# Kernel optimization log

Hardware: AMD Instinct MI355X
Metric: run time of the kernel (lower is better)

## Reference

```python
import jax, jax.numpy as jnp
import numpy as np

B, C, H, W = 32, 128, 64, 64
D = 256          # attn_unit_dim
FF = 512         # ffn latent dim (2.0 * 256, rounded to /16*16)
NL = 2           # n_attn_blocks
PH = PW = 2      # patch size
EPS = 1e-5


def _cf_ln(x, g, b):
    # channel-first LayerNorm over dim 1 (unbiased=False variance)
    m = jnp.mean(x, axis=1, keepdims=True)
    v = jnp.mean((x - m) ** 2, axis=1, keepdims=True)
    return (x - m) * jax.lax.rsqrt(v + EPS) * g.reshape(1, -1, 1, 1) + b.reshape(1, -1, 1, 1)


def _conv1x1(x, w, b=None):
    y = jnp.einsum('bcpq,dc->bdpq', x, w)
    return y if b is None else y + b.reshape(1, -1, 1, 1)


def _bn(x, g, b, m, v):
    # eval-mode BatchNorm2d with running stats
    return (x - m.reshape(1, -1, 1, 1)) * jax.lax.rsqrt(v.reshape(1, -1, 1, 1) + EPS) \
        * g.reshape(1, -1, 1, 1) + b.reshape(1, -1, 1, 1)


def setup_inputs() -> dict:
    key = jax.random.key(0)
    ks = iter(jax.random.split(key, 64))
    rn = lambda shape, s=0.02: jax.random.normal(next(ks), shape, jnp.float32) * s
    pv = lambda shape: 1.0 + 0.1 * jax.random.uniform(next(ks), shape, jnp.float32)
    return {
        'x': jax.random.normal(next(ks), (B, C, H, W), jnp.float32),
        # local_rep: depthwise 3x3 + BN + leaky_relu, then 1x1 -> D
        'dw_w': rn((C, 1, 3, 3), 0.1),
        'bn1_g': pv((C,)), 'bn1_b': rn((C,), 0.1),
        'bn1_m': rn((C,), 0.1), 'bn1_v': pv((C,)),
        'c1_w': rn((D, C)), 'c1_b': rn((D,), 0.01),
        # per-layer transformer params (stacked over NL)
        'ln1_g': pv((NL, D)), 'ln1_b': rn((NL, D), 0.1),
        'qkv_w': rn((NL, 1 + 2 * D, D)), 'qkv_b': rn((NL, 1 + 2 * D), 0.01),
        'out_w': rn((NL, D, D)), 'out_b': rn((NL, D), 0.01),
        'ln2_g': pv((NL, D)), 'ln2_b': rn((NL, D), 0.1),
        'f1_w': rn((NL, FF, D)), 'f1_b': rn((NL, FF), 0.01),
        'f2_w': rn((NL, D, FF)), 'f2_b': rn((NL, D), 0.01),
        'lnf_g': pv((D,)), 'lnf_b': rn((D,), 0.1),
        # conv_proj: 1x1 (no bias) + BN
        'proj_w': rn((C, D)),
        'bn2_g': pv((C,)), 'bn2_b': rn((C,), 0.1),
        'bn2_m': rn((C,), 0.1), 'bn2_v': pv((C,)),
    }


def reference(x, dw_w, bn1_g, bn1_b, bn1_m, bn1_v, c1_w, c1_b,
              ln1_g, ln1_b, qkv_w, qkv_b, out_w, out_b,
              ln2_g, ln2_b, f1_w, f1_b, f2_w, f2_b,
              lnf_g, lnf_b, proj_w, bn2_g, bn2_b, bn2_m, bn2_v):
    # local representation: depthwise 3x3 conv + BN + leaky_relu(0.1) + 1x1 conv
    y = jax.lax.conv_general_dilated(
        x, dw_w, window_strides=(1, 1), padding=[(1, 1), (1, 1)],
        dimension_numbers=('NCHW', 'OIHW', 'NCHW'), feature_group_count=C)
    y = _bn(y, bn1_g, bn1_b, bn1_m, bn1_v)
    y = jax.nn.leaky_relu(y, 0.1)
    y = _conv1x1(y, c1_w, c1_b)                       # [B, D, H, W]

    # unfold -> [B, D, P, N], P = PH*PW pixels/patch, N = patches
    nh, nw = H // PH, W // PW
    p = y.reshape(B, D, nh, PH, nw, PW).transpose(0, 1, 3, 5, 2, 4).reshape(B, D, PH * PW, nh * nw)

    # global representation: NL pre-norm linear-attention transformer blocks
    for l in range(NL):
        z = _cf_ln(p, ln1_g[l], ln1_b[l])
        qkv = _conv1x1(z, qkv_w[l], qkv_b[l])          # [B, 1+2D, P, N]
        q, k, v = qkv[:, :1], qkv[:, 1:1 + D], qkv[:, 1 + D:]
        scores = jax.nn.softmax(q, axis=-1)            # softmax over patches N
        ctx = jnp.sum(k * scores, axis=-1, keepdims=True)  # [B, D, P, 1]
        attn = _conv1x1(jax.nn.relu(v) * ctx, out_w[l], out_b[l])
        p = p + attn
        z = _cf_ln(p, ln2_g[l], ln2_b[l])
        h = jax.nn.leaky_relu(_conv1x1(z, f1_w[l], f1_b[l]), 0.1)
        p = p + _conv1x1(h, f2_w[l], f2_b[l])
    p = _cf_ln(p, lnf_g, lnf_b)

    # fold back -> [B, D, H, W]
    fm = p.reshape(B, D, PH, PW, nh, nw).transpose(0, 1, 4, 2, 5, 3).reshape(B, D, H, W)

    # conv_proj: 1x1 (no bias) + BN -> [B, C, H, W]
    fm = _conv1x1(fm, proj_w)
    fm = _bn(fm, bn2_g, bn2_b, bn2_m, bn2_v)
    return fm
```

## Files before the change

### kernel.cpp

```cpp
#include <hip/hip_runtime.h>


typedef short  bh8 __attribute__((ext_vector_type(8)));
typedef float  f4  __attribute__((ext_vector_type(4)));
typedef unsigned short us2 __attribute__((ext_vector_type(2)));
typedef unsigned short us4 __attribute__((ext_vector_type(4)));

constexpr int Bc = 32, Cc = 128, Dc = 256, FFc = 512;
constexpr int NNc = 1024, Sc = 4096;
constexpr float EPSc = 1e-5f;

enum SrcMode { S_LNF32, S_BF16 };
enum OutMode { O_STOREF32, O_FOLDBN };

__device__ __forceinline__ unsigned short f2bf(float f) {
  union { float f; unsigned int u; } v; v.f = f;
  unsigned int u = v.u + 0x7FFFu + ((v.u >> 16) & 1u);
  return (unsigned short)(u >> 16);
}

__global__ __launch_bounds__(256) void k_wconv(
    const float* __restrict__ w, unsigned short* __restrict__ dst,
    int total, int klog2)
{
  int idx = blockIdx.x * 256 + threadIdx.x;
  if (idx >= total) return;
  int K = 1 << klog2;
  int m = idx >> klog2, k = idx & (K - 1);
  int Mt = total >> klog2;
  size_t a = ((size_t)((k >> 5) * (Mt >> 4) + (m >> 4)) * 64
              + (((k >> 3) & 3) << 4) + (m & 15)) * 8 + (k & 7);
  dst[a] = f2bf(w[idx]);
}

__global__ __launch_bounds__(256) void k_dwconv(
    const float* __restrict__ x, const float* __restrict__ dww,
    const float* __restrict__ g, const float* __restrict__ bb,
    const float* __restrict__ mm, const float* __restrict__ vv,
    unsigned short* __restrict__ y1)
{
  int idx = blockIdx.x * 256 + threadIdx.x;
  int w4 = (idx & 15) * 4;
  int h  = (idx >> 4) & 63;
  int c  = (idx >> 10) & 127;
  int bi = idx >> 17;
  const float* xb = x + (size_t)(bi * 128 + c) * Sc;
  const float* wp = dww + c * 9;
  float acc[4] = {0.f, 0.f, 0.f, 0.f};
  #pragma unroll
  for (int kh = 0; kh < 3; ++kh) {
    int rr = h + kh - 1;
    if (rr < 0 || rr > 63) continue;
    const float* row = xb + rr * 64;
    float4 m4 = *reinterpret_cast<const float4*>(row + w4);
    float v[6];
    v[0] = (w4 > 0)  ? row[w4 - 1] : 0.f;
    v[1] = m4.x; v[2] = m4.y; v[3] = m4.z; v[4] = m4.w;
    v[5] = (w4 < 60) ? row[w4 + 4] : 0.f;
    float w0 = wp[kh * 3], w1 = wp[kh * 3 + 1], w2 = wp[kh * 3 + 2];
    #pragma unroll
    for (int o = 0; o < 4; ++o)
      acc[o] += w0 * v[o] + w1 * v[o + 1] + w2 * v[o + 2];
  }
  float sc = g[c] * rsqrtf(vv[c] + EPSc);
  float sh = bb[c] - mm[c] * sc;
  unsigned short r[4];
  #pragma unroll
  for (int o = 0; o < 4; ++o) {
    float val = acc[o] * sc + sh;
    r[o] = f2bf(val > 0.f ? val : 0.1f * val);
  }
  int ph = h & 1;
  size_t base = (size_t)(bi * 128 + c) * Sc + (h >> 1) * 32 + (w4 >> 1);
  *reinterpret_cast<us2*>(y1 + base + (ph * 2 + 0) * NNc) = (us2){r[0], r[2]};
  *reinterpret_cast<us2*>(y1 + base + (ph * 2 + 1) * NNc) = (us2){r[1], r[3]};
}

template<bool QD>
__global__ __launch_bounds__(256) void k_lnstats(
    const float* __restrict__ p, const float* __restrict__ wgq,
    float* __restrict__ mean_, float* __restrict__ rstd_, float* __restrict__ qdot)
{
  __shared__ float wg_s[256];
  int t = threadIdx.x;
  if (QD) { wg_s[t] = wgq[t]; __syncthreads(); }
  int pos = blockIdx.x * 256 + t;
  int b = pos >> 12, s = pos & 4095;
  const float* base = p + (size_t)b * Dc * Sc + s;
  float sum = 0.f, sq = 0.f, qa = 0.f;
  for (int d = 0; d < Dc; ++d) {
    float v = base[(size_t)d * Sc];
    sum += v; sq += v * v;
    if (QD) qa += v * wg_s[d];
  }
  float m   = sum * (1.f / Dc);
  float var = sq * (1.f / Dc) - m * m;
  mean_[pos] = m;
  rstd_[pos] = rsqrtf(fmaxf(var, 0.f) + EPSc);
  if (QD) qdot[pos] = qa;
}

__global__ void k_prep(const float* __restrict__ wq, const float* __restrict__ lng,
                       const float* __restrict__ lnb, const float* __restrict__ qb,
                       float* __restrict__ wgq, float* __restrict__ scal)
{
  int t = threadIdx.x, lane = t & 63, wv = t >> 6;
  float w = wq[t];
  float a = w * lng[t], c2 = w * lnb[t];
  wgq[t] = a;
  __shared__ float ra[4], rb[4];
  #pragma unroll
  for (int off = 32; off > 0; off >>= 1) { a += __shfl_xor(a, off); c2 += __shfl_xor(c2, off); }
  if (lane == 0) { ra[wv] = a; rb[wv] = c2; }
  __syncthreads();
  if (t == 0) {
    scal[0] = ra[0] + ra[1] + ra[2] + ra[3];
    scal[1] = rb[0] + rb[1] + rb[2] + rb[3] + qb[0];
  }
}

__global__ __launch_bounds__(256) void k_softmax2(
    const float* __restrict__ qdot, const float* __restrict__ mean_,
    const float* __restrict__ rstd_, const float* __restrict__ scal,
    float* __restrict__ ub, float* __restrict__ Ub)
{
  int bp = blockIdx.x, b = bp >> 2, pp = bp & 3;
  int t = threadIdx.x, lane = t & 63, wv = t >> 6;
  __shared__ float r3[4], r4[4];
  float s1 = scal[0], s2 = scal[1];
  int pos0 = b * Sc + pp * NNc;
  float q[4], m_r[4], rs_r[4];
  float mx = -3.4e38f;
  #pragma unroll
  for (int i = 0; i < 4; ++i) {
    int pos = pos0 + t + i * 256;
    m_r[i] = mean_[pos]; rs_r[i] = rstd_[pos];
    q[i] = rs_r[i] * qdot[pos] - m_r[i] * rs_r[i] * s1 + s2;
    mx = fmaxf(mx, q[i]);
  }
  #pragma unroll
  for (int off = 32; off > 0; off >>= 1) mx = fmaxf(mx, __shfl_xor(mx, off));
  if (lane == 0) r3[wv] = mx;
  __syncthreads();
  mx = fmaxf(fmaxf(r3[0], r3[1]), fmaxf(r3[2], r3[3]));
  float sum = 0.f;
  #pragma unroll
  for (int i = 0; i < 4; ++i) { q[i] = __expf(q[i] - mx); sum += q[i]; }
  #pragma unroll
  for (int off = 32; off > 0; off >>= 1) sum += __shfl_xor(sum, off);
  if (lane == 0) r4[wv] = sum;
  __syncthreads();
  float inv = 1.f / (r4[0] + r4[1] + r4[2] + r4[3]);
  float pU = 0.f;
  #pragma unroll
  for (int i = 0; i < 4; ++i) {
    float un = rs_r[i] * q[i] * inv;
    ub[(size_t)bp * NNc + t + i * 256] = un;
    pU += m_r[i] * un;
  }
  #pragma unroll
  for (int off = 32; off > 0; off >>= 1) pU += __shfl_xor(pU, off);
  if (lane == 0) r3[wv] = pU;
  __syncthreads();
  if (t == 0) Ub[bp] = r3[0] + r3[1] + r3[2] + r3[3];
}

__global__ __launch_bounds__(256) void k_tpass(
    const float* __restrict__ p, const float* __restrict__ ub,
    const float* __restrict__ Ub, const float* __restrict__ lng,
    const float* __restrict__ lnb, float* __restrict__ tb)
{
  int cs = blockIdx.x, pp = blockIdx.y, b = blockIdx.z;
  int bp = b * 4 + pp;
  int t = threadIdx.x, lane = t & 63, wv = t >> 6;
  __shared__ float u_s[1024];
  for (int i = t; i < 1024; i += 256) u_s[i] = ub[(size_t)bp * NNc + i];
  __syncthreads();
  float U = Ub[bp];
  const float* pb = p + (size_t)b * Dc * Sc + pp * NNc;
  for (int i = 0; i < 16; ++i) {
    int c = cs * 64 + wv * 16 + i;
    const float* row = pb + (size_t)c * Sc;
    float sm = 0.f;
    #pragma unroll
    for (int j = 0; j < 16; ++j) { int n = lane + 64 * j; sm += row[n] * u_s[n]; }
    #pragma unroll
    for (int off = 32; off > 0; off >>= 1) sm += __shfl_xor(sm, off);
    if (lane == 0) tb[(size_t)bp * Dc + c] = lng[c] * (sm - U) + lnb[c];
  }
}

__global__ __launch_bounds__(256) void k_ctx2(
    const float* __restrict__ tb, const float* __restrict__ wk,
    const float* __restrict__ bk, float* __restrict__ ctxb)
{
  int b = blockIdx.x, d = threadIdx.x;
  __shared__ float ts[4][256];
  for (int i = threadIdx.x; i < 1024; i += 256) ts[i >> 8][i & 255] = tb[(size_t)b * 1024 + i];
  __syncthreads();
  const float* wrow = wk + (size_t)d * 256;
  float bkd = bk[d];
  float accp[4] = {0.f, 0.f, 0.f, 0.f};
  for (int c = 0; c < 256; c += 4) {
    float4 wv = *reinterpret_cast<const float4*>(wrow + c);
    #pragma unroll
    for (int pp = 0; pp < 4; ++pp)
      accp[pp] += wv.x * ts[pp][c] + wv.y * ts[pp][c + 1]
                + wv.z * ts[pp][c + 2] + wv.w * ts[pp][c + 3];
  }
  #pragma unroll
  for (int pp = 0; pp < 4; ++pp)
    ctxb[((size_t)(b * 256 + d)) * 4 + pp] = accp[pp] + bkd;
}

__global__ void k_bn2pre(const float* __restrict__ g, const float* __restrict__ bb,
                         const float* __restrict__ mm, const float* __restrict__ vv,
                         float* __restrict__ sc, float* __restrict__ sh)
{
  int c = threadIdx.x;
  if (c < Cc) {
    float s = g[c] * rsqrtf(vv[c] + EPSc);
    sc[c] = s;
    sh[c] = bb[c] - mm[c] * s;
  }
}

template<int M1, bool ATTN, bool QDOT>
__global__ __launch_bounds__(256, 3) void k_fused(
    const float* __restrict__ p,
    const float* __restrict__ mean_, const float* __restrict__ rstd_,
    const float* __restrict__ lng, const float* __restrict__ lnb,
    const unsigned short* __restrict__ wf1, const float* __restrict__ b1,
    const float* __restrict__ ctxp,
    const unsigned short* __restrict__ wf2, const float* __restrict__ b2,
    float* __restrict__ dst,
    const float* __restrict__ wgq2,
    float* __restrict__ mean_o, float* __restrict__ rstd_o,
    float* __restrict__ qdot_o)
{
  constexpr int NT = 64;
  constexpr int NF = NT / 16;
  constexpr int SLABS = M1 / 128;
  int t = threadIdx.x;
  int wv = t >> 6, lane = t & 63;
  int q = lane >> 4, ln16 = lane & 15;
  int nt = blockIdx.x, pp = blockIdx.y, b = blockIdx.z;
  int n0 = nt * NT;

  __shared__ unsigned int At[256 * NT / 2];
  __shared__ unsigned short Frag[128 * NT];
  __shared__ float m_s[NT], rs_s[NT];
  __shared__ float ctx_s[ATTN ? 256 : 4];

  size_t pbase = (size_t)b * Dc * Sc + pp * NNc + n0;

  int kp_s = (t >> 5) & 7;
  int col  = (t & 31) * 2;

  auto kof = [&](int it) { return ((it >> 1) << 5) + ((it & 1) << 4) + kp_s * 2; };

  int ka = kof(0), kb = kof(1);
  float2 a0 = *reinterpret_cast<const float2*>(p + pbase + (size_t)ka * Sc + col);
  float2 a1 = *reinterpret_cast<const float2*>(p + pbase + (size_t)(ka + 1) * Sc + col);
  float2 b0 = *reinterpret_cast<const float2*>(p + pbase + (size_t)kb * Sc + col);
  float2 b1v = *reinterpret_cast<const float2*>(p + pbase + (size_t)(kb + 1) * Sc + col);

  if (t < NT) {
    int pos = b * Sc + pp * NNc + n0 + t;
    m_s[t]  = mean_[pos];
    rs_s[t] = rstd_[pos];
  }
  if (ATTN) ctx_s[t] = ctxp[(size_t)(b * Dc + t) * 4 + pp];
  __syncthreads();

  float ms0 = m_s[col], rs0 = rs_s[col];
  float ms1 = m_s[col + 1], rs1 = rs_s[col + 1];

  auto wrA = [&](int k0, int cx, unsigned int pk) {
    At[(((k0 >> 5) * 4 + (cx >> 4)) << 8) + ((((k0 >> 3) & 3) * 16 + (cx & 15)) << 2)
       + ((k0 & 7) >> 1)] = pk;
  };

  #pragma unroll 2
  for (int it = 0; it < 16; it += 2) {
    {
      int k0 = kof(it);
      float g0 = lng[k0], g1 = lng[k0 + 1];
      float h0 = lnb[k0], h1 = lnb[k0 + 1];
      float v00 = (a0.x - ms0) * rs0 * g0 + h0;
      float v01 = (a0.y - ms1) * rs1 * g0 + h0;
      float v10 = (a1.x - ms0) * rs0 * g1 + h1;
      float v11 = (a1.y - ms1) * rs1 * g1 + h1;
      if (it + 2 < 16) {
        int kn = kof(it + 2);
        a0 = *reinterpret_cast<const float2*>(p + pbase + (size_t)kn * Sc + col);
        a1 = *reinterpret_cast<const float2*>(p + pbase + (size_t)(kn + 1) * Sc + col);
      }
      wrA(k0, col,     (unsigned int)f2bf(v00) | ((unsigned int)f2bf(v10) << 16));
      wrA(k0, col + 1, (unsigned int)f2bf(v01) | ((unsigned int)f2bf(v11) << 16));
    }
    {
      int k0 = kof(it + 1);
      float g0 = lng[k0], g1 = lng[k0 + 1];
      float h0 = lnb[k0], h1 = lnb[k0 + 1];
      float v00 = (b0.x - ms0) * rs0 * g0 + h0;
      float v01 = (b0.y - ms1) * rs1 * g0 + h0;
      float v10 = (b1v.x - ms0) * rs0 * g1 + h1;
      float v11 = (b1v.y - ms1) * rs1 * g1 + h1;
      if (it + 3 < 16) {
        int kn = kof(it + 3);
        b0  = *reinterpret_cast<const float2*>(p + pbase + (size_t)kn * Sc + col);
        b1v = *reinterpret_cast<const float2*>(p + pbase + (size_t)(kn + 1) * Sc + col);
      }
      wrA(k0, col,     (unsigned int)f2bf(v00) | ((unsigned int)f2bf(v10) << 16));
      wrA(k0, col + 1, (unsigned int)f2bf(v01) | ((unsigned int)f2bf(v11) << 16));
    }
  }
  __syncthreads();

  const unsigned short* Ats = (const unsigned short*)At;

  f4 acc2[4][NF];
  #pragma unroll
  for (int i = 0; i < 4; ++i)
    #pragma unroll
    for (int j = 0; j < NF; ++j) acc2[i][j] = (f4){0.f, 0.f, 0.f, 0.f};

  for (int s = 0; s < SLABS; ++s) {
    f4 acc1[2][NF];
    #pragma unroll
    for (int i = 0; i < 2; ++i)
      #pragma unroll
      for (int j = 0; j < NF; ++j) acc1[i][j] = (f4){0.f, 0.f, 0.f, 0.f};

    for (int kc = 0; kc < 256; kc += 32) {
      bh8 aw[2];
      #pragma unroll
      for (int tm = 0; tm < 2; ++tm)
        aw[tm] = *(const bh8*)(wf1 + ((size_t)((kc >> 5) * (M1 >> 4) + s * 8 + wv * 2 + tm) * 64 + lane) * 8);
      #pragma unroll
      for (int tn = 0; tn < NF; ++tn) {
        bh8 bwf = *(const bh8*)(Ats + ((kc >> 5) * 4 + tn) * 512 + lane * 8);
        #pragma unroll
        for (int tm = 0; tm < 2; ++tm)
          acc1[tm][tn] = __builtin_amdgcn_mfma_f32_16x16x32_bf16(aw[tm], bwf, acc1[tm][tn], 0, 0, 0);
      }
    }

    __syncthreads();

    #pragma unroll
    for (int tm = 0; tm < 2; ++tm) {
      int row0l = wv * 32 + tm * 16 + q * 4;
      int row0g = s * 128 + row0l;
      float bia[4], cxv[4];
      #pragma unroll
      for (int r = 0; r < 4; ++r) {
        bia[r] = b1[row0g + r];
        if (ATTN) cxv[r] = ctx_s[row0g + r];
      }
      int kt2 = row0l >> 5;
      int sub = (row0l >> 3) & 3;
      int jo  = row0l & 7;
      #pragma unroll
      for (int tn = 0; tn < NF; ++tn) {
        int cl = tn * 16 + ln16;
        us4 pk;
        #pragma unroll
        for (int r = 0; r < 4; ++r) {
          float v = acc1[tm][tn][r] + bia[r];
          if (ATTN) v = fmaxf(v, 0.f) * cxv[r];
          else      v = v > 0.f ? v : 0.1f * v;
          pk[r] = f2bf(v);
        }
        *reinterpret_cast<us4*>(Frag + (((kt2 * 4 + (cl >> 4)) * 64 + ((sub << 4) | (cl & 15))) * 8 + jo)) = pk;
      }
    }
    __syncthreads();

    for (int kc2 = 0; kc2 < 4; ++kc2) {
      bh8 aw2[4];
      #pragma unroll
      for (int tm = 0; tm < 4; ++tm)
        aw2[tm] = *(const bh8*)(wf2 + ((size_t)((s * 4 + kc2) * 16 + wv * 4 + tm) * 64 + lane) * 8);
      #pragma unroll
      for (int tn = 0; tn < NF; ++tn) {
        bh8 bwf = *(const bh8*)(Frag + ((kc2 * 4 + tn) * 512) + lane * 8);
        #pragma unroll
        for (int tm = 0; tm < 4; ++tm)
          acc2[tm][tn] = __builtin_amdgcn_mfma_f32_16x16x32_bf16(aw2[tm], bwf, acc2[tm][tn], 0, 0, 0);
      }
    }
  }

  float s1[NF], s2[NF], s3[NF];
  #pragma unroll
  for (int tn = 0; tn < NF; ++tn) { s1[tn] = 0.f; s2[tn] = 0.f; s3[tn] = 0.f; }
  #pragma unroll
  for (int tm = 0; tm < 4; ++tm) {
    #pragma unroll
    for (int r = 0; r < 4; ++r) {
      int row = wv * 64 + tm * 16 + q * 4 + r;
      float bv = b2[row];
      float wqr = QDOT ? wgq2[row] : 0.f;
      #pragma unroll
      for (int tn = 0; tn < NF; ++tn) {
        int cx = n0 + tn * 16 + ln16;
        size_t da = (size_t)(b * Dc + row) * Sc + pp * NNc + cx;
        float v = dst[da] + acc2[tm][tn][r] + bv;
        dst[da] = v;
        s1[tn] += v; s2[tn] += v * v;
        if (QDOT) s3[tn] += v * wqr;
      }
    }
  }
  #pragma unroll
  for (int tn = 0; tn < NF; ++tn) {
    s1[tn] += __shfl_xor(s1[tn], 16); s1[tn] += __shfl_xor(s1[tn], 32);
    s2[tn] += __shfl_xor(s2[tn], 16); s2[tn] += __shfl_xor(s2[tn], 32);
    if (QDOT) { s3[tn] += __shfl_xor(s3[tn], 16); s3[tn] += __shfl_xor(s3[tn], 32); }
  }
  __syncthreads();
  float* fr = (float*)Frag;
  if (q == 0) {
    #pragma unroll
    for (int tn = 0; tn < NF; ++tn) {
      int cx = tn * 16 + ln16;
      fr[(wv * 3 + 0) * NT + cx] = s1[tn];
      fr[(wv * 3 + 1) * NT + cx] = s2[tn];
      fr[(wv * 3 + 2) * NT + cx] = s3[tn];
    }
  }
  __syncthreads();
  if (t < NT) {
    float a1s = 0.f, a2s = 0.f, a3s = 0.f;
    #pragma unroll
    for (int w2 = 0; w2 < 4; ++w2) {
      a1s += fr[(w2 * 3 + 0) * NT + t];
      a2s += fr[(w2 * 3 + 1) * NT + t];
      a3s += fr[(w2 * 3 + 2) * NT + t];
    }
    int pos = b * Sc + pp * NNc + n0 + t;
    float mn  = a1s * (1.f / 256.f);
    float var = a2s * (1.f / 256.f) - mn * mn;
    mean_o[pos] = mn;
    rstd_o[pos] = rsqrtf(fmaxf(var, 0.f) + EPSc);
    if (QDOT) qdot_o[pos] = a3s;
  }
}

template<int KTOT, int MTOT, int SRCCH, int SSTR, bool SPP,
         SrcMode SM, OutMode OM>
__global__ __launch_bounds__(256) void k_mm(
    const void* __restrict__ src,
    const float* __restrict__ mean_, const float* __restrict__ rstd_,
    const float* __restrict__ lng, const float* __restrict__ lnb,
    const unsigned short* __restrict__ wf, const float* __restrict__ bias,
    const float* __restrict__ bnsc, const float* __restrict__ bnsh,
    void* __restrict__ dst)
{
  int t = threadIdx.x;
  int wv = t >> 6, lane = t & 63;
  int wm = wv & 1, wn = wv >> 1;
  int q = lane >> 4, ln16 = lane & 15;
  int nb = blockIdx.x, b = blockIdx.z;
  int pp = blockIdx.y & 3, mb = blockIdx.y >> 2;
  int n0  = nb * 128;
  int MB0 = mb * 128;

  __shared__ unsigned int Alds[128 * 20];
  __shared__ float m_s[128], rs_s[128];

  if (SM == S_LNF32 && t < 128) {
    int pos = b * Sc + pp * NNc + n0 + t;
    m_s[t]  = mean_[pos];
    rs_s[t] = rstd_[pos];
  }

  f4 acc[4][4];
  #pragma unroll
  for (int i = 0; i < 4; ++i)
    #pragma unroll
    for (int j = 0; j < 4; ++j) acc[i][j] = (f4){0.f, 0.f, 0.f, 0.f};

  size_t sbase = (size_t)b * SRCCH * SSTR + pp * NNc + n0;
  int mtb = (MB0 >> 4) + wm * 4;

  for (int kc = 0; kc < KTOT; kc += 32) {
    bh8 aw[4];
    #pragma unroll
    for (int tm = 0; tm < 4; ++tm)
      aw[tm] = *(const bh8*)(wf + ((size_t)((kc >> 5) * (MTOT >> 4) + mtb + tm) * 64 + lane) * 8);
    __syncthreads();
    #pragma unroll
    for (int it = 0; it < 8; ++it) {
      int n_l = (t & 63) + (it & 1) * 64;
      int kp  = (t >> 6) + (it >> 1) * 4;
      int k0  = kc + kp * 2;
      unsigned int pk;
      if (SM == S_LNF32) {
        const float* sp = (const float*)src;
        float a0 = sp[sbase + (size_t)k0 * SSTR + n_l];
        float a1 = sp[sbase + (size_t)(k0 + 1) * SSTR + n_l];
        float ms = m_s[n_l], rs = rs_s[n_l];
        a0 = (a0 - ms) * rs * lng[k0] + lnb[k0];
        a1 = (a1 - ms) * rs * lng[k0 + 1] + lnb[k0 + 1];
        pk = (unsigned int)f2bf(a0) | ((unsigned int)f2bf(a1) << 16);
      } else {
        const unsigned short* sp = (const unsigned short*)src;
        unsigned int u0 = sp[sbase + (size_t)k0 * SSTR + n_l];
        unsigned int u1 = sp[sbase + (size_t)(k0 + 1) * SSTR + n_l];
        pk = u0 | (u1 << 16);
      }
      Alds[n_l * 20 + kp] = pk;
    }
    __syncthreads();
    const unsigned short* al = (const unsigned short*)Alds;
    #pragma unroll
    for (int tn = 0; tn < 4; ++tn) {
      int nrow = wn * 64 + tn * 16 + ln16;
      bh8 bwf = *(const bh8*)(al + nrow * 40 + q * 8);
      #pragma unroll
      for (int tm = 0; tm < 4; ++tm)
        acc[tm][tn] = __builtin_amdgcn_mfma_f32_16x16x32_bf16(aw[tm], bwf, acc[tm][tn], 0, 0, 0);
    }
  }

  #pragma unroll
  for (int tm = 0; tm < 4; ++tm) {
    #pragma unroll
    for (int r = 0; r < 4; ++r) {
      int row = MB0 + wm * 64 + tm * 16 + q * 4 + r;
      float scv = 0.f, shv = 0.f, bv = 0.f;
      if (OM == O_FOLDBN) { scv = bnsc[row]; shv = bnsh[row]; }
      else                { bv = bias[row]; }
      #pragma unroll
      for (int tn = 0; tn < 4; ++tn) {
        int col = n0 + wn * 64 + tn * 16 + ln16;
        float v = acc[tm][tn][r];
        if (OM == O_FOLDBN) {
          int hh = 2 * (col >> 5) + (pp >> 1), ww = 2 * (col & 31) + (pp & 1);
          ((float*)dst)[((size_t)(b * Cc + row)) * Sc + hh * 64 + ww] = v * scv + shv;
        } else {
          ((float*)dst)[(size_t)(b * MTOT + row) * Sc + pp * NNc + col] = v + bv;
        }
      }
    }
  }
}

extern "C" void kernel_launch(void* const* d_in, const int* in_sizes, int n_in,
                              void* d_out, int out_size, void* d_ws, size_t ws_size,
                              hipStream_t stream)
{
  const float* x     = (const float*)d_in[0];
  const float* dw_w  = (const float*)d_in[1];
  const float* bn1_g = (const float*)d_in[2];
  const float* bn1_b = (const float*)d_in[3];
  const float* bn1_m = (const float*)d_in[4];
  const float* bn1_v = (const float*)d_in[5];
  const float* c1_w  = (const float*)d_in[6];
  const float* c1_b  = (const float*)d_in[7];
  const float* ln1_g = (const float*)d_in[8];
  const float* ln1_b = (const float*)d_in[9];
  const float* qkv_w = (const float*)d_in[10];
  const float* qkv_b = (const float*)d_in[11];
  const float* out_w = (const float*)d_in[12];
  const float* out_b = (const float*)d_in[13];
  const float* ln2_g = (const float*)d_in[14];
  const float* ln2_b = (const float*)d_in[15];
  const float* f1_w  = (const float*)d_in[16];
  const float* f1_b  = (const float*)d_in[17];
  const float* f2_w  = (const float*)d_in[18];
  const float* f2_b  = (const float*)d_in[19];
  const float* lnf_g = (const float*)d_in[20];
  const float* lnf_b = (const float*)d_in[21];
  const float* projw = (const float*)d_in[22];
  const float* bn2_g = (const float*)d_in[23];
  const float* bn2_b = (const float*)d_in[24];
  const float* bn2_m = (const float*)d_in[25];
  const float* bn2_v = (const float*)d_in[26];
  float* out = (float*)d_out;

  float* ws    = (float*)d_ws;
  float* p     = ws;
  float* reg   = p + (size_t)33554432;
  unsigned short* y1u = (unsigned short*)reg;
  float* mean2 = reg;
  float* rstd2 = reg + 131072;
  float* meanb = reg   + (size_t)8388608;
  float* rstdb = meanb + 131072;
  float* qdotb = rstdb + 131072;
  float* ub    = qdotb + 131072;
  float* Ub    = ub    + 131072;
  float* tb    = Ub    + 128;
  float* ctxb  = tb    + 32768;
  float* wgq   = ctxb  + 32768;
  float* scal  = wgq   + 512;
  float* bnscb = scal  + 16;
  float* bnshb = bnscb + 128;
  unsigned short* wfb = (unsigned short*)(bnshb + 128);
  unsigned short* wf_c1   = wfb;
  unsigned short* wf_v0   = wfb + 32768;
  unsigned short* wf_proj = wfb + 32768 + 2 * 393216;

  k_wconv<<<128, 256, 0, stream>>>(c1_w, wf_c1, 256 * 128, 7);
  for (int l = 0; l < 2; ++l) {
    const float* wvp = qkv_w + ((size_t)l * 513 + 257) * Dc;
    unsigned short* base = wf_v0 + (size_t)l * 393216;
    k_wconv<<<256, 256, 0, stream>>>(wvp, base, 256 * 256, 8);
    k_wconv<<<256, 256, 0, stream>>>(out_w + (size_t)l * Dc * Dc, base + 65536, 256 * 256, 8);
    k_wconv<<<512, 256, 0, stream>>>(f1_w + (size_t)l * FFc * Dc, base + 131072, 512 * 256, 8);
    k_wconv<<<512, 256, 0, stream>>>(f2_w + (size_t)l * Dc * FFc, base + 262144, 256 * 512, 9);
  }
  k_wconv<<<128, 256, 0, stream>>>(projw, wf_proj, 128 * 256, 8);

  for (int l = 0; l < 2; ++l)
    k_prep<<<1, 256, 0, stream>>>(qkv_w + (size_t)l * 513 * Dc,
                                  ln1_g + l * Dc, ln1_b + l * Dc,
                                  qkv_b + l * 513, wgq + l * 256, scal + l * 2);

  k_dwconv<<<16384, 256, 0, stream>>>(x, dw_w, bn1_g, bn1_b, bn1_m, bn1_v, y1u);

  k_mm<128, 256, 128, 4096, true, S_BF16, O_STOREF32>
      <<<dim3(8, 8, 32), 256, 0, stream>>>(
      y1u, nullptr, nullptr, nullptr, nullptr, wf_c1, c1_b, nullptr, nullptr, p);

  k_lnstats<true><<<512, 256, 0, stream>>>(p, wgq, meanb, rstdb, qdotb);

  for (int l = 0; l < 2; ++l) {
    const float* g1 = ln1_g + l * Dc; const float* b1 = ln1_b + l * Dc;
    const float* g2 = ln2_g + l * Dc; const float* b2 = ln2_b + l * Dc;
    const float* wk = qkv_w + ((size_t)l * 513 + 1) * Dc;
    const float* bk = qkv_b + l * 513 + 1;
    const float* bvv = qkv_b + l * 513 + 257;
    unsigned short* wbase = wf_v0 + (size_t)l * 393216;

    k_softmax2<<<128, 256, 0, stream>>>(qdotb, meanb, rstdb, scal + l * 2, ub, Ub);
    k_tpass<<<dim3(4, 4, 32), 256, 0, stream>>>(p, ub, Ub, g1, b1, tb);
    k_ctx2<<<32, 256, 0, stream>>>(tb, wk, bk, ctxb);

    k_fused<256, true, false><<<dim3(16, 4, 32), 256, 0, stream>>>(
        p, meanb, rstdb, g1, b1, wbase, bvv, ctxb,
        wbase + 65536, out_b + l * Dc, p,
        nullptr, mean2, rstd2, nullptr);

    if (l == 0) {
      k_fused<512, false, true><<<dim3(16, 4, 32), 256, 0, stream>>>(
          p, mean2, rstd2, g2, b2, wbase + 131072, f1_b + l * FFc, nullptr,
          wbase + 262144, f2_b + l * Dc, p,
          wgq + 256, meanb, rstdb, qdotb);
    } else {
      k_fused<512, false, false><<<dim3(16, 4, 32), 256, 0, stream>>>(
          p, mean2, rstd2, g2, b2, wbase + 131072, f1_b + l * FFc, nullptr,
          wbase + 262144, f2_b + l * Dc, p,
          nullptr, meanb, rstdb, nullptr);
    }
  }

  k_bn2pre<<<1, 128, 0, stream>>>(bn2_g, bn2_b, bn2_m, bn2_v, bnscb, bnshb);
  k_mm<256, 128, 256, 4096, true, S_LNF32, O_FOLDBN>
      <<<dim3(8, 4, 32), 256, 0, stream>>>(
      p, meanb, rstdb, lnf_g, lnf_b, wf_proj, nullptr, bnscb, bnshb, out);
}
```

Measured before the change: 878.3 us.

## Use 512-thread blocks in fused MLP kernel and prefetch residual early

Doubles the fused attention/FFN kernel's block to 8 waves. Each wave now owns half as many output rows in both GEMMs, and the layernorm staging loop runs half as many iterations per thread. The residual values from p are loaded into registers before the GEMM loop, so the epilogue no longer does a read-modify-write from global memory. This is meant to raise waves per CU and hide latency. In exchange, the block needs more barrier participation, the cross-wave reduction grows to 8 partials, and holding the residuals adds register pressure.

```diff
diff --git a/kernel.cpp b/kernel.cpp
--- a/kernel.cpp
+++ b/kernel.cpp
@@ -226,7 +226,7 @@
 }
 
 template<int M1, bool ATTN, bool QDOT>
-__global__ __launch_bounds__(256, 3) void k_fused(
+__global__ __launch_bounds__(512, 4) void k_fused(
     const float* __restrict__ p,
     const float* __restrict__ mean_, const float* __restrict__ rstd_,
     const float* __restrict__ lng, const float* __restrict__ lnb,
@@ -254,10 +254,10 @@
 
   size_t pbase = (size_t)b * Dc * Sc + pp * NNc + n0;
 
-  int kp_s = (t >> 5) & 7;
+  int kp_s = t >> 5;
   int col  = (t & 31) * 2;
 
-  auto kof = [&](int it) { return ((it >> 1) << 5) + ((it & 1) << 4) + kp_s * 2; };
+  auto kof = [&](int it) { return (it << 5) + kp_s * 2; };
 
   int ka = kof(0), kb = kof(1);
   float2 a0 = *reinterpret_cast<const float2*>(p + pbase + (size_t)ka * Sc + col);
@@ -270,7 +270,7 @@
     m_s[t]  = mean_[pos];
     rs_s[t] = rstd_[pos];
   }
-  if (ATTN) ctx_s[t] = ctxp[(size_t)(b * Dc + t) * 4 + pp];
+  if (ATTN && t < 256) ctx_s[t] = ctxp[(size_t)(b * Dc + t) * 4 + pp];
   __syncthreads();
 
   float ms0 = m_s[col], rs0 = rs_s[col];
@@ -281,8 +281,8 @@
        + ((k0 & 7) >> 1)] = pk;
   };
 
-  #pragma unroll 2
-  for (int it = 0; it < 16; it += 2) {
+  #pragma unroll
+  for (int it = 0; it < 8; it += 2) {
     {
       int k0 = kof(it);
       float g0 = lng[k0], g1 = lng[k0 + 1];
@@ -291,7 +291,7 @@
       float v01 = (a0.y - ms1) * rs1 * g0 + h0;
       float v10 = (a1.x - ms0) * rs0 * g1 + h1;
       float v11 = (a1.y - ms1) * rs1 * g1 + h1;
-      if (it + 2 < 16) {
+      if (it + 2 < 8) {
         int kn = kof(it + 2);
         a0 = *reinterpret_cast<const float2*>(p + pbase + (size_t)kn * Sc + col);
         a1 = *reinterpret_cast<const float2*>(p + pbase + (size_t)(kn + 1) * Sc + col);
@@ -307,7 +307,7 @@
       float v01 = (b0.y - ms1) * rs1 * g0 + h0;
       float v10 = (b1v.x - ms0) * rs0 * g1 + h1;
       float v11 = (b1v.y - ms1) * rs1 * g1 + h1;
-      if (it + 3 < 16) {
+      if (it + 3 < 8) {
         int kn = kof(it + 3);
         b0  = *reinterpret_cast<const float2*>(p + pbase + (size_t)kn * Sc + col);
         b1v = *reinterpret_cast<const float2*>(p + pbase + (size_t)(kn + 1) * Sc + col);
@@ -318,40 +318,43 @@
   }
   __syncthreads();
 
+  float res[2][4][4];
+  #pragma unroll
+  for (int tm = 0; tm < 2; ++tm)
+    #pragma unroll
+    for (int r = 0; r < 4; ++r) {
+      int row = wv * 32 + tm * 16 + q * 4 + r;
+      #pragma unroll
+      for (int tn = 0; tn < NF; ++tn)
+        res[tm][r][tn] = dst[pbase + (size_t)row * Sc + tn * 16 + ln16];
+    }
+
   const unsigned short* Ats = (const unsigned short*)At;
 
-  f4 acc2[4][NF];
-  #pragma unroll
-  for (int i = 0; i < 4; ++i)
+  f4 acc2[2][NF];
+  #pragma unroll
+  for (int i = 0; i < 2; ++i)
     #pragma unroll
     for (int j = 0; j < NF; ++j) acc2[i][j] = (f4){0.f, 0.f, 0.f, 0.f};
 
   for (int s = 0; s < SLABS; ++s) {
-    f4 acc1[2][NF];
-    #pragma unroll
-    for (int i = 0; i < 2; ++i)
-      #pragma unroll
-      for (int j = 0; j < NF; ++j) acc1[i][j] = (f4){0.f, 0.f, 0.f, 0.f};
+    f4 acc1[NF];
+    #pragma unroll
+    for (int j = 0; j < NF; ++j) acc1[j] = (f4){0.f, 0.f, 0.f, 0.f};
 
     for (int kc = 0; kc < 256; kc += 32) {
-      bh8 aw[2];
-      #pragma unroll
-      for (int tm = 0; tm < 2; ++tm)
-        aw[tm] = *(const bh8*)(wf1 + ((size_t)((kc >> 5) * (M1 >> 4) + s * 8 + wv * 2 + tm) * 64 + lane) * 8);
+      bh8 aw = *(const bh8*)(wf1 + ((size_t)((kc >> 5) * (M1 >> 4) + s * 8 + wv) * 64 + lane) * 8);
       #pragma unroll
       for (int tn = 0; tn < NF; ++tn) {
         bh8 bwf = *(const bh8*)(Ats + ((kc >> 5) * 4 + tn) * 512 + lane * 8);
-        #pragma unroll
-        for (int tm = 0; tm < 2; ++tm)
-          acc1[tm][tn] = __builtin_amdgcn_mfma_f32_16x16x32_bf16(aw[tm], bwf, acc1[tm][tn], 0, 0, 0);
+        acc1[tn] = __builtin_amdgcn_mfma_f32_16x16x32_bf16(aw, bwf, acc1[tn], 0, 0, 0);
       }
     }
 
     __syncthreads();
 
-    #pragma unroll
-    for (int tm = 0; tm < 2; ++tm) {
-      int row0l = wv * 32 + tm * 16 + q * 4;
+    {
+      int row0l = wv * 16 + q * 4;
       int row0g = s * 128 + row0l;
       float bia[4], cxv[4];
       #pragma unroll
@@ -368,7 +371,7 @@
         us4 pk;
         #pragma unroll
         for (int r = 0; r < 4; ++r) {
-          float v = acc1[tm][tn][r] + bia[r];
+          float v = acc1[tn][r] + bia[r];
           if (ATTN) v = fmaxf(v, 0.f) * cxv[r];
           else      v = v > 0.f ? v : 0.1f * v;
           pk[r] = f2bf(v);
@@ -379,15 +382,15 @@
     __syncthreads();
 
     for (int kc2 = 0; kc2 < 4; ++kc2) {
-      bh8 aw2[4];
-      #pragma unroll
-      for (int tm = 0; tm < 4; ++tm)
-        aw2[tm] = *(const bh8*)(wf2 + ((size_t)((s * 4 + kc2) * 16 + wv * 4 + tm) * 64 + lane) * 8);
+      bh8 aw2[2];
+      #pragma unroll
+      for (int tm = 0; tm < 2; ++tm)
+        aw2[tm] = *(const bh8*)(wf2 + ((size_t)((s * 4 + kc2) * 16 + wv * 2 + tm) * 64 + lane) * 8);
       #pragma unroll
       for (int tn = 0; tn < NF; ++tn) {
         bh8 bwf = *(const bh8*)(Frag + ((kc2 * 4 + tn) * 512) + lane * 8);
         #pragma unroll
-        for (int tm = 0; tm < 4; ++tm)
+        for (int tm = 0; tm < 2; ++tm)
           acc2[tm][tn] = __builtin_amdgcn_mfma_f32_16x16x32_bf16(aw2[tm], bwf, acc2[tm][tn], 0, 0, 0);
       }
     }
@@ -397,18 +400,16 @@
   #pragma unroll
   for (int tn = 0; tn < NF; ++tn) { s1[tn] = 0.f; s2[tn] = 0.f; s3[tn] = 0.f; }
   #pragma unroll
-  for (int tm = 0; tm < 4; ++tm) {
+  for (int tm = 0; tm < 2; ++tm) {
     #pragma unroll
     for (int r = 0; r < 4; ++r) {
-      int row = wv * 64 + tm * 16 + q * 4 + r;
+      int row = wv * 32 + tm * 16 + q * 4 + r;
       float bv = b2[row];
       float wqr = QDOT ? wgq2[row] : 0.f;
       #pragma unroll
       for (int tn = 0; tn < NF; ++tn) {
-        int cx = n0 + tn * 16 + ln16;
-        size_t da = (size_t)(b * Dc + row) * Sc + pp * NNc + cx;
-        float v = dst[da] + acc2[tm][tn][r] + bv;
-        dst[da] = v;
+        float v = res[tm][r][tn] + acc2[tm][tn][r] + bv;
+        dst[pbase + (size_t)row * Sc + tn * 16 + ln16] = v;
         s1[tn] += v; s2[tn] += v * v;
         if (QDOT) s3[tn] += v * wqr;
       }
@@ -435,7 +436,7 @@
   if (t < NT) {
     float a1s = 0.f, a2s = 0.f, a3s = 0.f;
     #pragma unroll
-    for (int w2 = 0; w2 < 4; ++w2) {
+    for (int w2 = 0; w2 < 8; ++w2) {
       a1s += fr[(w2 * 3 + 0) * NT + t];
       a2s += fr[(w2 * 3 + 1) * NT + t];
       a3s += fr[(w2 * 3 + 2) * NT + t];
@@ -640,18 +641,18 @@
     k_tpass<<<dim3(4, 4, 32), 256, 0, stream>>>(p, ub, Ub, g1, b1, tb);
     k_ctx2<<<32, 256, 0, stream>>>(tb, wk, bk, ctxb);
 
-    k_fused<256, true, false><<<dim3(16, 4, 32), 256, 0, stream>>>(
+    k_fused<256, true, false><<<dim3(16, 4, 32), 512, 0, stream>>>(
         p, meanb, rstdb, g1, b1, wbase, bvv, ctxb,
         wbase + 65536, out_b + l * Dc, p,
         nullptr, mean2, rstd2, nullptr);
 
     if (l == 0) {
-      k_fused<512, false, true><<<dim3(16, 4, 32), 256, 0, stream>>>(
+      k_fused<512, false, true><<<dim3(16, 4, 32), 512, 0, stream>>>(
           p, mean2, rstd2, g2, b2, wbase + 131072, f1_b + l * FFc, nullptr,
           wbase + 262144, f2_b + l * Dc, p,
           wgq + 256, meanb, rstdb, qdotb);
     } else {
-      k_fused<512, false, false><<<dim3(16, 4, 32), 256, 0, stream>>>(
+      k_fused<512, false, false><<<dim3(16, 4, 32), 512, 0, stream>>>(
           p, mean2, rstd2, g2, b2, wbase + 131072, f1_b + l * FFc, nullptr,
           wbase + 262144, f2_b + l * Dc, p,
           nullptr, meanb, rstdb, nullptr);
```

Measured after the change: 884.3 us. No clear change (+0.7%).
